# Kernel optimization log

Measured on AMD Instinct MI355X. Metric: run time of the kernel, lower is better.

The kernel has to match this reference:

```python
import jax, jax.numpy as jnp
import numpy as np

B, N, H = 4, 256, 128
EPS_BN = 1e-5     # nn.BatchNorm default eps
EPS_AGG = 1e-20   # NodeFeatureLayer.epsilon


def _linear_params(key, fan_in, shape_w, shape_b):
    kw, kb = jax.random.split(key)
    bound = 1.0 / np.sqrt(fan_in)
    w = jax.random.uniform(kw, shape_w, minval=-bound, maxval=bound, dtype=jnp.float32)
    b = jax.random.uniform(kb, shape_b, minval=-bound, maxval=bound, dtype=jnp.float32)
    return w, b


def setup_inputs() -> dict:
    key = jax.random.key(0)
    ks = jax.random.split(key, 6)
    Ue_w, Ue_b = _linear_params(ks[2], H, (H, H), (H,))
    Ve_w, Ve_b = _linear_params(ks[3], H, (H, H), (H,))
    Un_w, Un_b = _linear_params(ks[4], H, (H, H), (H,))
    Vn_w, Vn_b = _linear_params(ks[5], H, (H, H), (H,))
    return {
        "x": jax.random.normal(ks[0], (B, N, H), dtype=jnp.float32),
        "e": jax.random.normal(ks[1], (B, N, N, H), dtype=jnp.float32),
        "Ue_w": Ue_w, "Ue_b": Ue_b,   # EdgeFeatureLayer.U
        "Ve_w": Ve_w, "Ve_b": Ve_b,   # EdgeFeatureLayer.V
        "Un_w": Un_w, "Un_b": Un_b,   # NodeFeatureLayer.U
        "Vn_w": Vn_w, "Vn_b": Vn_b,   # NodeFeatureLayer.V
        "bn_x_g": jnp.ones((H,), jnp.float32), "bn_x_b": jnp.zeros((H,), jnp.float32),
        "bn_e_g": jnp.ones((H,), jnp.float32), "bn_e_b": jnp.zeros((H,), jnp.float32),
    }


def _bn(t, gamma, beta, axes):
    # BatchNorm with track_running_stats=False: normalize per-channel (last dim)
    # over all other axes using batch statistics (biased variance).
    m = jnp.mean(t, axis=axes, keepdims=True)
    v = jnp.var(t, axis=axes, keepdims=True)
    return (t - m) * jax.lax.rsqrt(v + EPS_BN) * gamma + beta


def reference(x, e, Ue_w, Ue_b, Ve_w, Ve_b, Un_w, Un_b, Vn_w, Vn_b,
              bn_x_g, bn_x_b, bn_e_g, bn_e_b):
    # EdgeFeatureLayer: Ue + Vx_rows + Vx_cols  -> (B,N,N,H)
    Vx = x @ Ve_w.T + Ve_b                       # (B,N,H)
    e_feat = (e @ Ue_w.T + Ue_b
              + Vx[:, :, None, :]                # rows: unsqueeze(2)
              + Vx[:, None, :, :])               # cols: unsqueeze(1)
    gates = jax.nn.sigmoid(e_feat)               # (B,N,N,H)

    # NodeFeatureLayer: Ux + sum_j(gate_ij * Vx_j) / (eps + sum_j gate_ij)
    Vnx = x @ Vn_w.T + Vn_b                      # (B,N,H)
    num = jnp.einsum('bijh,bjh->bih', gates, Vnx)
    den = EPS_AGG + jnp.sum(gates, axis=2)       # (B,N,H)
    x_feat = x @ Un_w.T + Un_b + num / den

    # norm -> (no dropout) -> relu -> residual
    x_new = x + jax.nn.relu(_bn(x_feat, bn_x_g, bn_x_b, (0, 1)))
    e_new = e + jax.nn.relu(_bn(e_feat, bn_e_g, bn_e_b, (0, 1, 2)))
    return (x_new, e_new)
```

## Files before the change

### kernel.cpp

```cpp
#include <hip/hip_runtime.h>
#include <math.h>

typedef short bf16x8 __attribute__((ext_vector_type(8)));
typedef float f32x4 __attribute__((ext_vector_type(4)));

#define BB 4
#define NN 256
#define HH 128
#define ME_ (BB*NN*NN)

#define VX_OFF   0
#define UX_OFF   131072
#define VXN_OFF  262144
#define NUM_OFF  393216
#define DEN_OFF  655360
#define PSUM_OFF 917504
#define PSQ_OFF  1179648
#define XF_OFF   1441792
#define PSR_OFF  1572864
#define PSQR_OFF 1581056
#define PSX_OFF  1589248
#define PSXX_OFF 1597440
#define SCE_OFF  1605632
#define SHE_OFF  1605760
#define SCX_OFF  1605888
#define SHX_OFF  1606016
#define W16_OFF  1606144

__device__ inline short f2bf(float f) {
    unsigned u = __builtin_bit_cast(unsigned, f);
    u += 0x7FFFu + ((u >> 16) & 1u);
    return (short)(u >> 16);
}
__device__ inline float bfbits2f(unsigned hi) {
    return __builtin_bit_cast(float, hi);
}

__global__ __launch_bounds__(256) void k_prep(const float* __restrict__ W,
                                              unsigned short* __restrict__ W16)
{
    int i = blockIdx.x * 256 + threadIdx.x;
    W16[i] = (unsigned short)f2bf(W[i]);
}

__global__ __launch_bounds__(256) void k_linx(
    const float* __restrict__ x,
    const float* __restrict__ Ve_w, const float* __restrict__ Ve_b,
    const float* __restrict__ Vn_w, const float* __restrict__ Vn_b,
    const float* __restrict__ Un_w, const float* __restrict__ Un_b,
    float* ws)
{
    __shared__ float xs[8 * 128];
    int t = threadIdx.x;
    int rowbase = blockIdx.x * 8;

    const float4* xg = (const float4*)(x + (size_t)rowbase * 128);
    ((float4*)xs)[t] = xg[t];
    __syncthreads();

    int h = t & 127, rh = t >> 7;
    float accV[4], accN[4], accU[4];
    float bV = Ve_b[h], bN = Vn_b[h], bU = Un_b[h];
    #pragma unroll
    for (int q = 0; q < 4; ++q) { accV[q] = bV; accN[q] = bN; accU[q] = bU; }

    const float4* wV = (const float4*)(Ve_w + (size_t)h * 128);
    const float4* wN = (const float4*)(Vn_w + (size_t)h * 128);
    const float4* wU = (const float4*)(Un_w + (size_t)h * 128);

    #pragma unroll 4
    for (int k4 = 0; k4 < 32; ++k4) {
        float4 wv = wV[k4], wn = wN[k4], wu = wU[k4];
        #pragma unroll
        for (int q = 0; q < 4; ++q) {
            float4 xv = *(const float4*)&xs[(rh + 2 * q) * 128 + k4 * 4];
            accV[q] += xv.x*wv.x + xv.y*wv.y + xv.z*wv.z + xv.w*wv.w;
            accN[q] += xv.x*wn.x + xv.y*wn.y + xv.z*wn.z + xv.w*wn.w;
            accU[q] += xv.x*wu.x + xv.y*wu.y + xv.z*wu.z + xv.w*wu.w;
        }
    }
    unsigned* VXN = (unsigned*)(ws + VXN_OFF);
    #pragma unroll
    for (int q = 0; q < 4; ++q) {
        size_t idx = (size_t)(rowbase + rh + 2 * q) * 128 + h;
        ws[VX_OFF + idx] = accV[q];
        ws[UX_OFF + idx] = accU[q];
        VXN[idx] = ((unsigned)(unsigned short)f2bf(accV[q]))
                 | ((unsigned)(unsigned short)f2bf(accN[q]) << 16);
    }
}

__device__ inline void load_raw(const float* __restrict__ eb, int row, int g,
                                float4* raw)
{
    const float* rp = eb + (size_t)row * 128 + g * 8;
    #pragma unroll
    for (int kc = 0; kc < 4; ++kc) {
        raw[2*kc]   = *(const float4*)(rp + kc * 32);
        raw[2*kc+1] = *(const float4*)(rp + kc * 32 + 4);
    }
}
__device__ inline void cvt_frag(const float4* raw, bf16x8* afr)
{
    #pragma unroll
    for (int kc = 0; kc < 4; ++kc) {
        float4 f0 = raw[2*kc], f1 = raw[2*kc+1];
        bf16x8 a;
        a[0] = f2bf(f0.x); a[1] = f2bf(f0.y); a[2] = f2bf(f0.z); a[3] = f2bf(f0.w);
        a[4] = f2bf(f1.x); a[5] = f2bf(f1.y); a[6] = f2bf(f1.z); a[7] = f2bf(f1.w);
        afr[kc] = a;
    }
}
__device__ inline bf16x8 ldsW(const short* Wl, int h, int kc, int g, int swz)
{
    return *(const bf16x8*)((const char*)Wl + h * 256 + ((kc * 64 + g * 16) ^ swz));
}

__global__ __launch_bounds__(256, 3) void k_edge_stats(
    const float* __restrict__ e,
    const unsigned short* __restrict__ W16,
    const float* __restrict__ Ue_b,
    float* __restrict__ ws)
{
    __shared__ short Wl[16384];
    __shared__ float red[2048];
    int t   = threadIdx.x;
    int bx  = blockIdx.x;
    int bi  = bx >> 1, jh = bx & 1;
    int b   = bi >> 8;
    int wid = t >> 6, l = t & 63;
    int hsub = l & 15, g = l >> 4;
    int swz = (hsub & 7) << 4;
    int jbase = jh * 128 + wid * 32;

    const unsigned* VXNb = (const unsigned*)(ws + VXN_OFF) + (size_t)b * 32768;
    const float* eb = e + (size_t)bi * 32768;

    float4 raw[8];
    load_raw(eb, jbase + hsub, g, raw);
    unsigned pk_pre[4];
    #pragma unroll
    for (int r = 0; r < 4; ++r)
        pk_pre[r] = VXNb[(size_t)(jbase + g * 4 + r) * 128 + hsub];

    float biasv[8];
    #pragma unroll
    for (int ct = 0; ct < 8; ++ct) {
        int h = ct * 16 + hsub;
        biasv[ct] = Ue_b[h] + ws[VX_OFF + (size_t)bi * 128 + h];
    }

    const int4* Wg = (const int4*)W16;
    #pragma unroll
    for (int p = 0; p < 8; ++p) {
        int s = t + 256 * p;
        int r = s >> 4, c = s & 15;
        int addr = r * 256 + ((c * 16) ^ ((r & 7) << 4));
        *(int4*)((char*)Wl + addr) = Wg[s];
    }
    __syncthreads();

    float num[8] = {0,0,0,0,0,0,0,0}, den[8] = {0,0,0,0,0,0,0,0};
    float se[8]  = {0,0,0,0,0,0,0,0}, sq[8]  = {0,0,0,0,0,0,0,0};

    bf16x8 afr[4];

    #pragma unroll
    for (int rt = 0; rt < 2; ++rt) {
        int jb = jbase + rt * 16;
        cvt_frag(raw, afr);
        if (rt == 0) load_raw(eb, jbase + 16 + hsub, g, raw);

        unsigned pk_n[4];
        bf16x8 bfr_n[4];
        #pragma unroll
        for (int r = 0; r < 4; ++r)
            pk_n[r] = (rt == 0) ? pk_pre[r]
                                : VXNb[(size_t)(jb + g * 4 + r) * 128 + hsub];
        #pragma unroll
        for (int kc = 0; kc < 4; ++kc) bfr_n[kc] = ldsW(Wl, hsub, kc, g, swz);

        #pragma unroll
        for (int ct = 0; ct < 8; ++ct) {
            unsigned pk_c[4];
            bf16x8 bfr_c[4];
            #pragma unroll
            for (int r = 0; r < 4; ++r) pk_c[r] = pk_n[r];
            #pragma unroll
            for (int kc = 0; kc < 4; ++kc) bfr_c[kc] = bfr_n[kc];

            if (ct < 7) {
                int hn = (ct + 1) * 16 + hsub;
                #pragma unroll
                for (int r = 0; r < 4; ++r)
                    pk_n[r] = VXNb[(size_t)(jb + g * 4 + r) * 128 + hn];
                #pragma unroll
                for (int kc = 0; kc < 4; ++kc)
                    bfr_n[kc] = ldsW(Wl, hn, kc, g, swz);
            }

            f32x4 acc = {0.f, 0.f, 0.f, 0.f};
            #pragma unroll
            for (int kc = 0; kc < 4; ++kc)
                acc = __builtin_amdgcn_mfma_f32_16x16x32_bf16(afr[kc], bfr_c[kc], acc, 0, 0, 0);

            float bih = biasv[ct];
            #pragma unroll
            for (int r = 0; r < 4; ++r) {
                unsigned pk = pk_c[r];
                float vx  = bfbits2f(pk << 16);
                float vnx = bfbits2f(pk & 0xFFFF0000u);
                float v = acc[r] + bih + vx;
                float gv = 1.0f / (1.0f + __expf(-v));
                num[ct] += gv * vnx;
                den[ct] += gv;
                se[ct]  += v;
                sq[ct]  += v * v;
            }
        }
    }

    #pragma unroll
    for (int ct = 0; ct < 8; ++ct) {
        float n = num[ct], d = den[ct], s1 = se[ct], s2 = sq[ct];
        n  += __shfl_xor(n, 32);  n  += __shfl_xor(n, 16);
        d  += __shfl_xor(d, 32);  d  += __shfl_xor(d, 16);
        s1 += __shfl_xor(s1, 32); s1 += __shfl_xor(s1, 16);
        s2 += __shfl_xor(s2, 32); s2 += __shfl_xor(s2, 16);
        if (l < 16) {
            int h = ct * 16 + l;
            red[0 * 512 + wid * 128 + h] = n;
            red[1 * 512 + wid * 128 + h] = d;
            red[2 * 512 + wid * 128 + h] = s1;
            red[3 * 512 + wid * 128 + h] = s2;
        }
    }
    __syncthreads();
    if (t < 128) {
        int h = t;
        float sn = 0.f, sd = 0.f;
        #pragma unroll
        for (int w = 0; w < 4; ++w) {
            sn += red[0 * 512 + w * 128 + h];
            sd += red[1 * 512 + w * 128 + h];
        }
        ws[NUM_OFF + (size_t)bx * 128 + h] = sn;
        ws[DEN_OFF + (size_t)bx * 128 + h] = sd;
    } else {
        int h = t - 128;
        float s1 = 0.f, s2 = 0.f;
        #pragma unroll
        for (int w = 0; w < 4; ++w) {
            s1 += red[2 * 512 + w * 128 + h];
            s2 += red[3 * 512 + w * 128 + h];
        }
        ws[PSUM_OFF + (size_t)bx * 128 + h] = s1;
        ws[PSQ_OFF  + (size_t)bx * 128 + h] = s2;
    }
}

__global__ __launch_bounds__(256) void k_red(float* ws)
{
    __shared__ float sm[1024];
    int t = threadIdx.x, bid = blockIdx.x;
    int h = t & 127, p = t >> 7;

    float s1 = 0.f, s2 = 0.f;
    #pragma unroll
    for (int q = 0; q < 16; ++q) {
        size_t idx = (size_t)(bid * 32 + p * 16 + q) * 128 + h;
        s1 += ws[PSUM_OFF + idx];
        s2 += ws[PSQ_OFF + idx];
    }
    float sx = 0.f, sxx = 0.f;
    #pragma unroll
    for (int q = 0; q < 8; ++q) {
        int bi = bid * 16 + p * 8 + q;
        size_t i0 = (size_t)(2 * bi) * 128 + h, i1 = (size_t)(2 * bi + 1) * 128 + h;
        float nm = ws[NUM_OFF + i0] + ws[NUM_OFF + i1];
        float dn = 1e-20f + ws[DEN_OFF + i0] + ws[DEN_OFF + i1];
        float v = ws[UX_OFF + (size_t)bi * 128 + h] + nm / dn;
        ws[XF_OFF + (size_t)bi * 128 + h] = v;
        sx += v; sxx += v * v;
    }
    sm[0 * 256 + p * 128 + h] = s1;
    sm[1 * 256 + p * 128 + h] = s2;
    sm[2 * 256 + p * 128 + h] = sx;
    sm[3 * 256 + p * 128 + h] = sxx;
    __syncthreads();
    if (t < 128) {
        ws[PSR_OFF  + (size_t)bid * 128 + h] = sm[0*256 + h] + sm[0*256 + 128 + h];
        ws[PSQR_OFF + (size_t)bid * 128 + h] = sm[1*256 + h] + sm[1*256 + 128 + h];
    } else {
        ws[PSX_OFF  + (size_t)bid * 128 + h] = sm[2*256 + h] + sm[2*256 + 128 + h];
        ws[PSXX_OFF + (size_t)bid * 128 + h] = sm[3*256 + h] + sm[3*256 + 128 + h];
    }
}

__global__ __launch_bounds__(128) void k_fin(
    const float* __restrict__ bn_x_g, const float* __restrict__ bn_x_b,
    const float* __restrict__ bn_e_g, const float* __restrict__ bn_e_b,
    float* ws)
{
    int h = threadIdx.x;
    float s1 = 0.f, s2 = 0.f, sx = 0.f, sxx = 0.f;
    for (int r = 0; r < 64; ++r) {
        size_t idx = (size_t)r * 128 + h;
        s1 += ws[PSR_OFF + idx];
        s2 += ws[PSQR_OFF + idx];
        sx += ws[PSX_OFF + idx];
        sxx+= ws[PSXX_OFF + idx];
    }
    float me = s1 / (float)ME_;
    float ve = s2 / (float)ME_ - me * me;
    float sce = bn_e_g[h] * rsqrtf(ve + 1e-5f);
    ws[SCE_OFF + h] = sce;
    ws[SHE_OFF + h] = bn_e_b[h] - me * sce;
    float mx = sx / 1024.0f;
    float vx = sxx / 1024.0f - mx * mx;
    float scx = bn_x_g[h] * rsqrtf(vx + 1e-5f);
    ws[SCX_OFF + h] = scx;
    ws[SHX_OFF + h] = bn_x_b[h] - mx * scx;
}

__global__ __launch_bounds__(256) void k_xnew(
    const float* __restrict__ x, const float* __restrict__ ws,
    float* __restrict__ out_x)
{
    __shared__ float sc[128], sh[128];
    int t = threadIdx.x;
    if (t < 128) sc[t] = ws[SCX_OFF + t];
    else         sh[t - 128] = ws[SHX_OFF + t - 128];
    __syncthreads();

    int i4 = blockIdx.x * 256 + t;
    int hb = (i4 & 31) * 4;
    float4 scv = *(const float4*)&sc[hb];
    float4 shv = *(const float4*)&sh[hb];
    float4 xf = ((const float4*)(ws + XF_OFF))[i4];
    float4 xv = ((const float4*)x)[i4];
    float4 o;
    o.x = xv.x + fmaxf(xf.x * scv.x + shv.x, 0.0f);
    o.y = xv.y + fmaxf(xf.y * scv.y + shv.y, 0.0f);
    o.z = xv.z + fmaxf(xf.z * scv.z + shv.z, 0.0f);
    o.w = xv.w + fmaxf(xf.w * scv.w + shv.w, 0.0f);
    ((float4*)out_x)[i4] = o;
}

__global__ __launch_bounds__(256, 3) void k_edge_apply(
    const float* __restrict__ e,
    const unsigned short* __restrict__ W16,
    const float* __restrict__ Ue_b,
    const float* __restrict__ ws,
    float* __restrict__ out_e)
{
    __shared__ short Wl[16384];
    int t   = threadIdx.x;
    int bx  = blockIdx.x;
    int bi  = bx >> 1, jh = bx & 1;
    int b   = bi >> 8;
    int wid = t >> 6, l = t & 63;
    int hsub = l & 15, g = l >> 4;
    int swz = (hsub & 7) << 4;
    int jbase = jh * 128 + wid * 32;

    const float* VXf  = ws + VX_OFF + (size_t)b * 32768;
    const float* eb   = e     + (size_t)bi * 32768;
    float*       oute = out_e + (size_t)bi * 32768;

    float4 raw[8];
    load_raw(eb, jbase + hsub, g, raw);
    float vx_pre[4], er_pre[4];
    #pragma unroll
    for (int r = 0; r < 4; ++r) {
        size_t idx = (size_t)(jbase + g * 4 + r) * 128 + hsub;
        vx_pre[r] = VXf[idx];
        er_pre[r] = eb[idx];
    }
    float biasv[8], sceR[8], sheR[8];
    #pragma unroll
    for (int ct = 0; ct < 8; ++ct) {
        int h = ct * 16 + hsub;
        biasv[ct] = Ue_b[h] + ws[VX_OFF + (size_t)bi * 128 + h];
        sceR[ct]  = ws[SCE_OFF + h];
        sheR[ct]  = ws[SHE_OFF + h];
    }

    const int4* Wg = (const int4*)W16;
    #pragma unroll
    for (int p = 0; p < 8; ++p) {
        int s = t + 256 * p;
        int r = s >> 4, c = s & 15;
        int addr = r * 256 + ((c * 16) ^ ((r & 7) << 4));
        *(int4*)((char*)Wl + addr) = Wg[s];
    }
    __syncthreads();

    bf16x8 afr[4];

    #pragma unroll
    for (int rt = 0; rt < 2; ++rt) {
        int jb = jbase + rt * 16;
        cvt_frag(raw, afr);
        if (rt == 0) load_raw(eb, jbase + 16 + hsub, g, raw);

        float vx_n[4], er_n[4];
        bf16x8 bfr_n[4];
        #pragma unroll
        for (int r = 0; r < 4; ++r) {
            if (rt == 0) { vx_n[r] = vx_pre[r]; er_n[r] = er_pre[r]; }
            else {
                size_t idx = (size_t)(jb + g * 4 + r) * 128 + hsub;
                vx_n[r] = VXf[idx];
                er_n[r] = eb[idx];
            }
        }
        #pragma unroll
        for (int kc = 0; kc < 4; ++kc) bfr_n[kc] = ldsW(Wl, hsub, kc, g, swz);

        #pragma unroll
        for (int ct = 0; ct < 8; ++ct) {
            float vx_c[4], er_c[4];
            bf16x8 bfr_c[4];
            #pragma unroll
            for (int r = 0; r < 4; ++r) { vx_c[r] = vx_n[r]; er_c[r] = er_n[r]; }
            #pragma unroll
            for (int kc = 0; kc < 4; ++kc) bfr_c[kc] = bfr_n[kc];

            if (ct < 7) {
                int hn = (ct + 1) * 16 + hsub;
                #pragma unroll
                for (int r = 0; r < 4; ++r) {
                    size_t idx = (size_t)(jb + g * 4 + r) * 128 + hn;
                    vx_n[r] = VXf[idx];
                    er_n[r] = eb[idx];
                }
                #pragma unroll
                for (int kc = 0; kc < 4; ++kc)
                    bfr_n[kc] = ldsW(Wl, hn, kc, g, swz);
            }

            f32x4 acc = {0.f, 0.f, 0.f, 0.f};
            #pragma unroll
            for (int kc = 0; kc < 4; ++kc)
                acc = __builtin_amdgcn_mfma_f32_16x16x32_bf16(afr[kc], bfr_c[kc], acc, 0, 0, 0);

            float bih = biasv[ct], sc = sceR[ct], sh = sheR[ct];
            int h = ct * 16 + hsub;
            #pragma unroll
            for (int r = 0; r < 4; ++r) {
                int j = jb + g * 4 + r;
                float v = acc[r] + bih + vx_c[r];
                float f = v * sc + sh;
                oute[(size_t)j * 128 + h] = er_c[r] + fmaxf(f, 0.0f);
            }
        }
    }
}

extern "C" void kernel_launch(void* const* d_in, const int* in_sizes, int n_in,
                              void* d_out, int out_size, void* d_ws, size_t ws_size,
                              hipStream_t stream)
{
    const float* x      = (const float*)d_in[0];
    const float* e      = (const float*)d_in[1];
    const float* Ue_w   = (const float*)d_in[2];
    const float* Ue_b   = (const float*)d_in[3];
    const float* Ve_w   = (const float*)d_in[4];
    const float* Ve_b   = (const float*)d_in[5];
    const float* Un_w   = (const float*)d_in[6];
    const float* Un_b   = (const float*)d_in[7];
    const float* Vn_w   = (const float*)d_in[8];
    const float* Vn_b   = (const float*)d_in[9];
    const float* bn_x_g = (const float*)d_in[10];
    const float* bn_x_b = (const float*)d_in[11];
    const float* bn_e_g = (const float*)d_in[12];
    const float* bn_e_b = (const float*)d_in[13];

    float* out   = (float*)d_out;
    float* out_x = out;
    float* out_e = out + 131072;
    float* ws    = (float*)d_ws;
    unsigned short* W16 = (unsigned short*)(ws + W16_OFF);

    k_prep       <<<64, 256, 0, stream>>>(Ue_w, W16);
    k_linx       <<<128, 256, 0, stream>>>(x, Ve_w, Ve_b, Vn_w, Vn_b, Un_w, Un_b, ws);
    k_edge_stats <<<2048, 256, 0, stream>>>(e, W16, Ue_b, ws);
    k_red        <<<64, 256, 0, stream>>>(ws);
    k_fin        <<<1, 128, 0, stream>>>(bn_x_g, bn_x_b, bn_e_g, bn_e_b, ws);
    k_xnew       <<<128, 256, 0, stream>>>(x, ws, out_x);
    k_edge_apply <<<2048, 256, 0, stream>>>(e, W16, Ue_b, ws, out_e);
}
```

Baseline: 139.2 us.

## Store Vx column tables transposed for vector loads and raise edge-kernel occupancy

k_linx now also writes transposed (h-major, j-contiguous) copies of Vx and the packed Vx/Vnx bf16 pair. The edge stats and apply kernels can then fetch the four j values a lane needs with a single 16-byte load instead of four scattered scalar loads. The aim is fewer memory instructions and less uncoalesced traffic in the gate computation. Launch-bound minimum occupancy is also raised (3→4 and 3→5), which constrains registers and risks spills.

```diff
diff --git a/kernel.cpp b/kernel.cpp
--- a/kernel.cpp
+++ b/kernel.cpp
@@ -11,21 +11,22 @@
 
 #define VX_OFF   0
 #define UX_OFF   131072
-#define VXN_OFF  262144
-#define NUM_OFF  393216
-#define DEN_OFF  655360
-#define PSUM_OFF 917504
-#define PSQ_OFF  1179648
-#define XF_OFF   1441792
-#define PSR_OFF  1572864
-#define PSQR_OFF 1581056
-#define PSX_OFF  1589248
-#define PSXX_OFF 1597440
-#define SCE_OFF  1605632
-#define SHE_OFF  1605760
-#define SCX_OFF  1605888
-#define SHX_OFF  1606016
-#define W16_OFF  1606144
+#define VXT_OFF  262144
+#define VXNT_OFF 393216
+#define NUM_OFF  524288
+#define DEN_OFF  786432
+#define PSUM_OFF 1048576
+#define PSQ_OFF  1310720
+#define XF_OFF   1572864
+#define PSR_OFF  1703936
+#define PSQR_OFF 1712128
+#define PSX_OFF  1720320
+#define PSXX_OFF 1728512
+#define SCE_OFF  1736704
+#define SHE_OFF  1736832
+#define SCX_OFF  1736960
+#define SHX_OFF  1737088
+#define W16_OFF  1737216
 
 __device__ inline short f2bf(float f) {
     unsigned u = __builtin_bit_cast(unsigned, f);
@@ -79,14 +80,19 @@
             accU[q] += xv.x*wu.x + xv.y*wu.y + xv.z*wu.z + xv.w*wu.w;
         }
     }
-    unsigned* VXN = (unsigned*)(ws + VXN_OFF);
+    float* VXT = ws + VXT_OFF;
+    unsigned* VXNT = (unsigned*)(ws + VXNT_OFF);
     #pragma unroll
     for (int q = 0; q < 4; ++q) {
-        size_t idx = (size_t)(rowbase + rh + 2 * q) * 128 + h;
+        int row = rowbase + rh + 2 * q;
+        size_t idx = (size_t)row * 128 + h;
         ws[VX_OFF + idx] = accV[q];
         ws[UX_OFF + idx] = accU[q];
-        VXN[idx] = ((unsigned)(unsigned short)f2bf(accV[q]))
-                 | ((unsigned)(unsigned short)f2bf(accN[q]) << 16);
+        int bb = row >> 8, jj = row & 255;
+        size_t tidx = (size_t)bb * 32768 + (size_t)h * 256 + jj;
+        VXT[tidx] = accV[q];
+        VXNT[tidx] = ((unsigned)(unsigned short)f2bf(accV[q]))
+                   | ((unsigned)(unsigned short)f2bf(accN[q]) << 16);
     }
 }
 
@@ -116,7 +122,7 @@
     return *(const bf16x8*)((const char*)Wl + h * 256 + ((kc * 64 + g * 16) ^ swz));
 }
 
-__global__ __launch_bounds__(256, 3) void k_edge_stats(
+__global__ __launch_bounds__(256, 4) void k_edge_stats(
     const float* __restrict__ e,
     const unsigned short* __restrict__ W16,
     const float* __restrict__ Ue_b,
@@ -133,15 +139,13 @@
     int swz = (hsub & 7) << 4;
     int jbase = jh * 128 + wid * 32;
 
-    const unsigned* VXNb = (const unsigned*)(ws + VXN_OFF) + (size_t)b * 32768;
+    const uint4* VXNT4 = (const uint4*)((const unsigned*)(ws + VXNT_OFF)
+                                        + (size_t)b * 32768);
     const float* eb = e + (size_t)bi * 32768;
 
     float4 raw[8];
     load_raw(eb, jbase + hsub, g, raw);
-    unsigned pk_pre[4];
-    #pragma unroll
-    for (int r = 0; r < 4; ++r)
-        pk_pre[r] = VXNb[(size_t)(jbase + g * 4 + r) * 128 + hsub];
+    uint4 pk_pre = VXNT4[(size_t)hsub * 64 + (jbase >> 2) + g];
 
     float biasv[8];
     #pragma unroll
@@ -171,29 +175,22 @@
         cvt_frag(raw, afr);
         if (rt == 0) load_raw(eb, jbase + 16 + hsub, g, raw);
 
-        unsigned pk_n[4];
+        uint4 pk_n = (rt == 0) ? pk_pre
+                               : VXNT4[(size_t)hsub * 64 + (jb >> 2) + g];
         bf16x8 bfr_n[4];
         #pragma unroll
-        for (int r = 0; r < 4; ++r)
-            pk_n[r] = (rt == 0) ? pk_pre[r]
-                                : VXNb[(size_t)(jb + g * 4 + r) * 128 + hsub];
-        #pragma unroll
         for (int kc = 0; kc < 4; ++kc) bfr_n[kc] = ldsW(Wl, hsub, kc, g, swz);
 
         #pragma unroll
         for (int ct = 0; ct < 8; ++ct) {
-            unsigned pk_c[4];
+            uint4 pk_c = pk_n;
             bf16x8 bfr_c[4];
-            #pragma unroll
-            for (int r = 0; r < 4; ++r) pk_c[r] = pk_n[r];
             #pragma unroll
             for (int kc = 0; kc < 4; ++kc) bfr_c[kc] = bfr_n[kc];
 
             if (ct < 7) {
                 int hn = (ct + 1) * 16 + hsub;
-                #pragma unroll
-                for (int r = 0; r < 4; ++r)
-                    pk_n[r] = VXNb[(size_t)(jb + g * 4 + r) * 128 + hn];
+                pk_n = VXNT4[(size_t)hn * 64 + (jb >> 2) + g];
                 #pragma unroll
                 for (int kc = 0; kc < 4; ++kc)
                     bfr_n[kc] = ldsW(Wl, hn, kc, g, swz);
@@ -207,7 +204,7 @@
             float bih = biasv[ct];
             #pragma unroll
             for (int r = 0; r < 4; ++r) {
-                unsigned pk = pk_c[r];
+                unsigned pk = (&pk_c.x)[r];
                 float vx  = bfbits2f(pk << 16);
                 float vnx = bfbits2f(pk & 0xFFFF0000u);
                 float v = acc[r] + bih + vx;
@@ -347,7 +344,7 @@
     ((float4*)out_x)[i4] = o;
 }
 
-__global__ __launch_bounds__(256, 3) void k_edge_apply(
+__global__ __launch_bounds__(256, 5) void k_edge_apply(
     const float* __restrict__ e,
     const unsigned short* __restrict__ W16,
     const float* __restrict__ Ue_b,
@@ -364,19 +361,18 @@
     int swz = (hsub & 7) << 4;
     int jbase = jh * 128 + wid * 32;
 
-    const float* VXf  = ws + VX_OFF + (size_t)b * 32768;
+    const float4* VXT4 = (const float4*)(ws + VXT_OFF + (size_t)b * 32768);
     const float* eb   = e     + (size_t)bi * 32768;
     float*       oute = out_e + (size_t)bi * 32768;
 
     float4 raw[8];
     load_raw(eb, jbase + hsub, g, raw);
-    float vx_pre[4], er_pre[4];
-    #pragma unroll
-    for (int r = 0; r < 4; ++r) {
-        size_t idx = (size_t)(jbase + g * 4 + r) * 128 + hsub;
-        vx_pre[r] = VXf[idx];
-        er_pre[r] = eb[idx];
-    }
+    float4 vx_pre = VXT4[(size_t)hsub * 64 + (jbase >> 2) + g];
+    float er_pre[4];
+    #pragma unroll
+    for (int r = 0; r < 4; ++r)
+        er_pre[r] = eb[(size_t)(jbase + g * 4 + r) * 128 + hsub];
+
     float biasv[8], sceR[8], sheR[8];
     #pragma unroll
     for (int ct = 0; ct < 8; ++ct) {
@@ -404,37 +400,38 @@
         cvt_frag(raw, afr);
         if (rt == 0) load_raw(eb, jbase + 16 + hsub, g, raw);
 
-        float vx_n[4], er_n[4];
+        float4 vx_n;
+        float er_n[4];
         bf16x8 bfr_n[4];
-        #pragma unroll
-        for (int r = 0; r < 4; ++r) {
-            if (rt == 0) { vx_n[r] = vx_pre[r]; er_n[r] = er_pre[r]; }
-            else {
-                size_t idx = (size_t)(jb + g * 4 + r) * 128 + hsub;
-                vx_n[r] = VXf[idx];
-                er_n[r] = eb[idx];
-            }
+        if (rt == 0) {
+            vx_n = vx_pre;
+            #pragma unroll
+            for (int r = 0; r < 4; ++r) er_n[r] = er_pre[r];
+        } else {
+            vx_n = VXT4[(size_t)hsub * 64 + (jb >> 2) + g];
+            #pragma unroll
+            for (int r = 0; r < 4; ++r)
+                er_n[r] = eb[(size_t)(jb + g * 4 + r) * 128 + hsub];
         }
         #pragma unroll
         for (int kc = 0; kc < 4; ++kc) bfr_n[kc] = ldsW(Wl, hsub, kc, g, swz);
 
         #pragma unroll
         for (int ct = 0; ct < 8; ++ct) {
-            float vx_c[4], er_c[4];
+            float4 vx_c = vx_n;
+            float er_c[4];
             bf16x8 bfr_c[4];
             #pragma unroll
-            for (int r = 0; r < 4; ++r) { vx_c[r] = vx_n[r]; er_c[r] = er_n[r]; }
+            for (int r = 0; r < 4; ++r) er_c[r] = er_n[r];
             #pragma unroll
             for (int kc = 0; kc < 4; ++kc) bfr_c[kc] = bfr_n[kc];
 
             if (ct < 7) {
                 int hn = (ct + 1) * 16 + hsub;
+                vx_n = VXT4[(size_t)hn * 64 + (jb >> 2) + g];
                 #pragma unroll
-                for (int r = 0; r < 4; ++r) {
-                    size_t idx = (size_t)(jb + g * 4 + r) * 128 + hn;
-                    vx_n[r] = VXf[idx];
-                    er_n[r] = eb[idx];
-                }
+                for (int r = 0; r < 4; ++r)
+                    er_n[r] = eb[(size_t)(jb + g * 4 + r) * 128 + hn];
                 #pragma unroll
                 for (int kc = 0; kc < 4; ++kc)
                     bfr_n[kc] = ldsW(Wl, hn, kc, g, swz);
@@ -450,7 +447,7 @@
             #pragma unroll
             for (int r = 0; r < 4; ++r) {
                 int j = jb + g * 4 + r;
-                float v = acc[r] + bih + vx_c[r];
+                float v = acc[r] + bih + (&vx_c.x)[r];
                 float f = v * sc + sh;
                 oute[(size_t)j * 128 + h] = er_c[r] + fmaxf(f, 0.0f);
             }
```

Result: slower. 333.6 us (+139.6%).
